# Optimization experiments

Measured on AMD Instinct MI355X. Metric: run time of the kernel, lower is better.

## Reference

```python
import jax, jax.numpy as jnp
import numpy as np

KH, KW = 3, 3
DH, DW = 1, 1
H_OUT, W_OUT = 64, 64


def setup_inputs() -> dict:
    key = jax.random.key(0)
    k1, k2, k3 = jax.random.split(key, 3)
    x = jax.random.normal(k1, (32, 16, 66, 66), dtype=jnp.float32)
    # per-location (locally-connected) weights: [1, C_out, C_in, H_out, W_out, kh*kw]
    weight = jax.random.normal(k2, (1, 32, 16, 64, 64, 9), dtype=jnp.float32) * 0.1
    bias = jax.random.normal(k3, (1, 32, 64, 64), dtype=jnp.float32) * 0.1
    return {"x": x, "weight": weight, "bias": bias}


def _unfold(x):
    # torch x.unfold(2,kh,dh).unfold(3,kw,dw).view(B,C,Ho,Wo,kh*kw):
    # kernel index order is (i over kh, then j over kw).
    patches = jnp.stack(
        [x[:, :, i : i + H_OUT * DH : DH, j : j + W_OUT * DW : DW]
         for i in range(KH) for j in range(KW)],
        axis=-1,
    )  # [B, C_in, H_out, W_out, kh*kw]
    return patches


def reference(x, weight, bias):
    patches = _unfold(x)  # [B, C_in, Ho, Wo, K]
    # (x.unsqueeze(1) * weight).sum([2, -1]) == contraction over C_in and kernel,
    # with per-(h,w) unique weights; einsum avoids the huge 6D intermediate.
    out = jnp.einsum("bchwk,ochwk->bohw", patches, weight[0])
    out = out + bias  # bias has leading 1 batch dim, broadcasts
    return out
```

## Files before the change

### kernel.cpp

```cpp
#include <hip/hip_runtime.h>


#define CI_ 16
#define H_  64
#define W_  64
#define XW_ 66

typedef float f32x16 __attribute__((ext_vector_type(16)));
typedef short s16x8  __attribute__((ext_vector_type(8)));

__device__ inline short f2bf(float f) {
  unsigned u = __builtin_bit_cast(unsigned, f);
  u += 0x7fffu + ((u >> 16) & 1u);
  return (short)(u >> 16);
}

__global__ __launch_bounds__(256) void prep_x(const float* __restrict__ x,
                                              short* __restrict__ xP) {
  const int t = blockIdx.x * 256 + threadIdx.x;
  const int oct = t & 1;
  const int b   = (t >> 1) & 31;
  const int hhww = t >> 6;
  const float* sp = x + ((size_t)b * CI_ + oct * 8) * 4356 + hhww;
  s16x8 v;
#pragma unroll
  for (int e = 0; e < 8; ++e) v[e] = f2bf(sp[(size_t)e * 4356]);
  *(s16x8*)(xP + (size_t)t * 8) = v;
}

__global__ __launch_bounds__(256, 2) void lc2d_fused(
    const short* __restrict__ xP, const float* __restrict__ wt,
    const float* __restrict__ bias, float* __restrict__ out) {
  __shared__ short pw[4 * 9 * 32 * 16];

  const int d = blockIdx.x;
  const int L = (d & 7) * 128 + (d >> 3);
  const int wq = L & 15;
  const int h  = L >> 4;
  const int tx = threadIdx.x;
  const int w2 = threadIdx.y;
  const int tid = w2 * 64 + tx;
  const int ln   = tx & 31;
  const int half = tx >> 5;
  const int w = wq * 4 + w2;

  const short* ap0 = xP + ln * 16 + half * 8;
  s16x8 af[9];
#pragma unroll
  for (int kk = 0; kk < 9; ++kk) {
    const int i = kk / 3, j = kk - 3 * i;
    af[kk] = *(const s16x8*)(ap0 + (size_t)((h + i) * XW_ + (w + j)) * 512);
  }

  float4 vst[18];
#pragma unroll
  for (int i = 0; i < 18; ++i) {
    const int f4 = tid + 256 * i;
    const int seg = f4 / 9;
    const int q   = f4 % 9;
    vst[i] = ((const float4*)wt)[((size_t)seg * H_ + h) * 144 + wq * 9 + q];
  }

#pragma unroll
  for (int i = 0; i < 18; ++i) {
    const int f4 = tid + 256 * i;
    const int seg = f4 / 9;
    const int q   = f4 % 9;
    const int o  = seg >> 4;
    const int s3 = seg >> 3, s7 = seg & 7;
    const float* vv = (const float*)&vst[i];
#pragma unroll
    for (int e = 0; e < 4; ++e) {
      const int flat = 4 * q + e;
      const int k = flat - 9 * (flat / 9);
      const int g = ((flat << 6) + s3) ^ ((o ^ k) & 7);
      pw[(g << 3) | s7] = f2bf(vv[e]);
    }
  }
  __syncthreads();

  f32x16 acc = {0,0,0,0,0,0,0,0,0,0,0,0,0,0,0,0};
#pragma unroll
  for (int kk = 0; kk < 9; ++kk) {
    int g = ((w2 * 9 + kk) * 32 + ln) * 2 + half;
    g ^= (ln ^ kk) & 7;
    const s16x8 bf = *(const s16x8*)(pw + (g << 3));
    acc = __builtin_amdgcn_mfma_f32_32x32x16_bf16(af[kk], bf, acc, 0, 0, 0);
  }

  __syncthreads();
  float* tr = (float*)pw;
#pragma unroll
  for (int r = 0; r < 16; ++r) {
    const int b = (r & 3) + 8 * (r >> 2) + 4 * half;
    tr[(w2 * 32 + b) * 32 + ln] = acc[r];
  }
  __syncthreads();

  const int o = tid & 31;
  const int brow = tid >> 5;
  const float4 bv = *(const float4*)(bias + ((size_t)o * H_ + h) * W_ + wq * 4);
#pragma unroll
  for (int it = 0; it < 4; ++it) {
    const int b = it * 8 + brow;
    float4 v;
    v.x = tr[(0 * 32 + b) * 32 + o] + bv.x;
    v.y = tr[(1 * 32 + b) * 32 + o] + bv.y;
    v.z = tr[(2 * 32 + b) * 32 + o] + bv.z;
    v.w = tr[(3 * 32 + b) * 32 + o] + bv.w;
    *(float4*)(out + ((size_t)b * 32 + o) * (H_ * W_) + h * W_ + wq * 4) = v;
  }
}

__global__ __launch_bounds__(256, 4) void lc2d_mfma0(
    const float* __restrict__ xs, const float* __restrict__ wt,
    const float* __restrict__ bias, float* __restrict__ out) {
  __shared__ float wlds[8 * 32 * 36];
  const int d = blockIdx.x;
  const int L = (d & 7) * 128 + (d >> 3);
  const int wq = L & 15;
  const int h  = L >> 4;
  const int tx = threadIdx.x;
  const int w2 = threadIdx.y;
  const int ln = tx & 31;
  const int half = tx >> 5;
  const int tid = w2 * 64 + tx;
  const int w = wq * 4 + w2;
  f32x16 acc = {0,0,0,0,0,0,0,0,0,0,0,0,0,0,0,0};
  const int bbase = ln * 36 + w2 * 9;
  size_t abase = (size_t)ln * 69696 + (size_t)h * XW_ + w;

  for (int s = 0; s < 2; ++s) {
    const int c0 = s * 8;
    __syncthreads();
#pragma unroll
    for (int i = 0; i < 9; ++i) {
      const int f4 = tid + i * 256;
      const int cc = f4 / 288;
      const int rem = f4 - cc * 288;
      const int oo = rem / 9;
      const int q = rem - oo * 9;
      const float4* src = (const float4*)wt +
          (((size_t)oo * CI_ + (c0 + cc)) * H_ + h) * 144 + (size_t)wq * 9 + q;
      ((float4*)wlds)[f4] = *src;
    }
    __syncthreads();
#pragma unroll
    for (int cc = 0; cc < 8; ++cc) {
      const int c = c0 + cc;
      const float* ap = xs + abase + (size_t)c * 4356;
      float av[8] = {0,0,0,0,0,0,0,0};
      float bvv[8] = {0,0,0,0,0,0,0,0};
      av[0] = ap[half ? (2 * XW_ + 2) : 0];
      bvv[0] = wlds[cc * 1152 + bbase + (half ? 8 : 0)];
      if (half == 0) {
#pragma unroll
        for (int e = 1; e < 8; ++e) {
          const int i = e / 3, j = e - 3 * i;
          av[e] = ap[i * XW_ + j];
          bvv[e] = wlds[cc * 1152 + bbase + e];
        }
      }
      s16x8 afr, bfr;
#pragma unroll
      for (int e = 0; e < 8; ++e) { afr[e] = f2bf(av[e]); bfr[e] = f2bf(bvv[e]); }
      acc = __builtin_amdgcn_mfma_f32_32x32x16_bf16(afr, bfr, acc, 0, 0, 0);
    }
  }
  const float bvv = bias[((size_t)ln * H_ + h) * W_ + w];
#pragma unroll
  for (int r = 0; r < 16; ++r) {
    const int b = (r & 3) + 8 * (r >> 2) + 4 * half;
    out[(((size_t)b * 32 + ln) * H_ + h) * W_ + w] = acc[r] + bvv;
  }
}

extern "C" void kernel_launch(void* const* d_in, const int* in_sizes, int n_in,
                              void* d_out, int out_size, void* d_ws, size_t ws_size,
                              hipStream_t stream) {
  const float* x    = (const float*)d_in[0];
  const float* wt   = (const float*)d_in[1];
  const float* bias = (const float*)d_in[2];
  float* out = (float*)d_out;

  const size_t xp_bytes = (size_t)66 * 66 * 32 * 16 * sizeof(short);
  if (ws_size >= xp_bytes) {
    short* xP = (short*)d_ws;
    prep_x<<<1089, 256, 0, stream>>>(x, xP);
    lc2d_fused<<<1024, dim3(64, 4, 1), 0, stream>>>(xP, wt, bias, out);
  } else {
    lc2d_mfma0<<<1024, dim3(64, 4, 1), 0, stream>>>(x, wt, bias, out);
  }
}
```

Baseline: 39.95 us.

## Stage per-location weights into LDS via direct global-to-LDS loads as fp32

```diff
diff --git a/kernel.cpp b/kernel.cpp
--- a/kernel.cpp
+++ b/kernel.cpp
@@ -15,6 +15,12 @@
   return (short)(u >> 16);
 }
 
+__device__ inline void gload_lds16(const float* g, void* l) {
+  __builtin_amdgcn_global_load_lds(
+      (const __attribute__((address_space(1))) void*)g,
+      (__attribute__((address_space(3))) void*)l, 16, 0, 0);
+}
+
 __global__ __launch_bounds__(256) void prep_x(const float* __restrict__ x,
                                               short* __restrict__ xP) {
   const int t = blockIdx.x * 256 + threadIdx.x;
@@ -28,10 +34,10 @@
   *(s16x8*)(xP + (size_t)t * 8) = v;
 }
 
-__global__ __launch_bounds__(256, 2) void lc2d_fused(
+__global__ __launch_bounds__(256) void lc2d_fused(
     const short* __restrict__ xP, const float* __restrict__ wt,
     const float* __restrict__ bias, float* __restrict__ out) {
-  __shared__ short pw[4 * 9 * 32 * 16];
+  __shared__ float wlin[16 * 32 * 36];
 
   const int d = blockIdx.x;
   const int L = (d & 7) * 128 + (d >> 3);
@@ -52,44 +58,32 @@
     af[kk] = *(const s16x8*)(ap0 + (size_t)((h + i) * XW_ + (w + j)) * 512);
   }
 
-  float4 vst[18];
 #pragma unroll
   for (int i = 0; i < 18; ++i) {
-    const int f4 = tid + 256 * i;
-    const int seg = f4 / 9;
-    const int q   = f4 % 9;
-    vst[i] = ((const float4*)wt)[((size_t)seg * H_ + h) * 144 + wq * 9 + q];
-  }
-
-#pragma unroll
-  for (int i = 0; i < 18; ++i) {
-    const int f4 = tid + 256 * i;
-    const int seg = f4 / 9;
-    const int q   = f4 % 9;
-    const int o  = seg >> 4;
-    const int s3 = seg >> 3, s7 = seg & 7;
-    const float* vv = (const float*)&vst[i];
-#pragma unroll
-    for (int e = 0; e < 4; ++e) {
-      const int flat = 4 * q + e;
-      const int k = flat - 9 * (flat / 9);
-      const int g = ((flat << 6) + s3) ^ ((o ^ k) & 7);
-      pw[(g << 3) | s7] = f2bf(vv[e]);
-    }
+    const int G = i * 256 + tid;
+    const int segL = G / 9;
+    const int q    = G - 9 * segL;
+    const int o = segL & 31, c = segL >> 5;
+    const float* src = wt +
+        (((size_t)(o * 16 + c) * 9216 + (size_t)h * 144 + wq * 9 + q) << 2);
+    gload_lds16(src, (char*)wlin + (size_t)(i * 256 + w2 * 64) * 16);
   }
   __syncthreads();
 
   f32x16 acc = {0,0,0,0,0,0,0,0,0,0,0,0,0,0,0,0};
+  const int bbase = half * 9216 + ln * 36 + w2 * 9;
 #pragma unroll
   for (int kk = 0; kk < 9; ++kk) {
-    int g = ((w2 * 9 + kk) * 32 + ln) * 2 + half;
-    g ^= (ln ^ kk) & 7;
-    const s16x8 bf = *(const s16x8*)(pw + (g << 3));
+    s16x8 bf;
+#pragma unroll
+    for (int e = 0; e < 8; ++e) {
+      bf[e] = f2bf(wlin[bbase + e * 1152 + kk]);
+    }
     acc = __builtin_amdgcn_mfma_f32_32x32x16_bf16(af[kk], bf, acc, 0, 0, 0);
   }
 
   __syncthreads();
-  float* tr = (float*)pw;
+  float* tr = (float*)wlin;
 #pragma unroll
   for (int r = 0; r < 16; ++r) {
     const int b = (r & 3) + 8 * (r >> 2) + 4 * half;
```

Result: no change. 39.62 us (-0.8%).
